# Kernel tuning notes

Measured on AMD Instinct MI355X. Metric: run time of the kernel, lower is better.

The kernel has to match this reference:

```python
import jax, jax.numpy as jnp
import numpy as np

B, N = 16, 512


def _line_coords(n):
    # Discrete Fourier slice coordinates for all mValues (center=False, ridgelet=False).
    mu = n + n // 2 if n % 2 == 0 else n + 1
    p = 2 if n % 2 == 0 else n
    m = jnp.arange(mu)           # [mu]
    k = jnp.arange(n)            # [N]
    lt = (m < n)[:, None]        # m < N branch mask, [mu, 1]
    # m < N:  row = k,                 col = (k*m) % N
    # m >= N: row = (k*p*(m-N)) % N,   col = k
    row = jnp.where(lt, k[None, :], (k[None, :] * p * (m[:, None] - n)) % n)
    col = jnp.where(lt, (k[None, :] * m[:, None]) % n, k[None, :])
    return row, col  # each [mu, N] int32


def setup_inputs() -> dict:
    key = jax.random.key(0)
    return {"image": jax.random.normal(key, (B, N, N), dtype=jnp.float32)}


def reference(image):
    b, n, _ = image.shape
    row, col = _line_coords(n)                                   # [mu, N]
    dft = jnp.fft.fft2(image.astype(jnp.complex64), norm="ortho")  # [B, N, N] c64
    slices = dft[:, row, col]                                    # gather -> [B, mu, N]
    sino = jnp.fft.ifft(slices, norm="ortho")                    # [B, mu, N] c64
    # complex sinogram returned as stacked (real, imag) float channels
    return jnp.stack([sino.real, sino.imag], axis=-1)            # [B, mu, N, 2]
```

## Files before the change

### kernel.cpp

```cpp
#include <hip/hip_runtime.h>
#include <hip/hip_fp16.h>


#define NN 512
#define MU 768
#define MASK 511
#define SCALE 0.04419417382415922f
#define NB 768

typedef float v4f __attribute__((ext_vector_type(4)));

union H8 { float4 f4; __half2 h2[4]; };
union H4 { float2 f2; __half2 h2[2]; };

__device__ __forceinline__ void gridbar(unsigned* cnt, unsigned target) {
  __syncthreads();
  if (threadIdx.x == 0) {
    __threadfence();
    atomicAdd(cnt, 1u);
    while (__atomic_load_n(cnt, __ATOMIC_ACQUIRE) < target)
      __builtin_amdgcn_s_sleep(8);
    __threadfence();
  }
  __syncthreads();
}

__global__ __launch_bounds__(512, 6) void drt_fused(
    const float* __restrict__ img, float2* __restrict__ out,
    __half* __restrict__ A0, __half* __restrict__ B0,
    __half* __restrict__ A1, __half* __restrict__ B1,
    unsigned* __restrict__ bar) {
  __shared__ float LDS[8320];
  const int bid = blockIdx.x;
  const int t = threadIdx.x;

  if (bid < 512) {
    const int b = bid >> 5, tile = bid & 31;
    const int xt = tile & 7, wt = tile >> 3;
    const int x0 = xt * 64, w0 = wt * 64, x3 = ((xt + 4) & 7) * 64;
    const float* src = img + (size_t)b * NN * NN;
    float* TA = LDS;
    float* TB = LDS + 4160;
    for (int idx = t; idx < 4096; idx += 512) {
      int rr = idx >> 6, cc = idx & 63;
      TA[rr * 65 + cc] = src[(x0 + rr) * NN + w0 + cc];
      TB[rr * 65 + cc] = src[(x0 + rr) * NN + w0 + 256 + cc];
    }
    __syncthreads();
    __half2* d = (__half2*)A0 + (size_t)b * 512 * 256;
    for (int idx = t; idx < 2048; idx += 512) {
      int wl = idx >> 5, xp = idx & 31;
      float a0 = TA[(2 * xp) * 65 + wl] + TB[(2 * xp) * 65 + wl];
      float a1 = TA[(2 * xp + 1) * 65 + wl] + TB[(2 * xp + 1) * 65 + wl];
      d[(w0 + wl) * 256 + (x0 >> 1) + xp] = __float22half2_rn(make_float2(a0, a1));
    }
    __syncthreads();
    for (int idx = t; idx < 4096; idx += 512) {
      int rr = idx >> 6, cc = idx & 63;
      TB[rr * 65 + cc] = src[(x3 + rr) * NN + w0 + 256 + cc];
    }
    __syncthreads();
    for (int idx = t; idx < 2048; idx += 512) {
      int wl = idx >> 5, xp = idx & 31;
      float a0 = TA[(2 * xp) * 65 + wl] + TB[(2 * xp) * 65 + wl];
      float a1 = TA[(2 * xp + 1) * 65 + wl] + TB[(2 * xp + 1) * 65 + wl];
      d[(256 + w0 + wl) * 256 + (x0 >> 1) + xp] = __float22half2_rn(make_float2(a0, a1));
    }
  } else {
    const int v = bid - 512, b = v >> 4, unit = v & 15;
    const int w0 = unit * 16;
    const float2* s2 = (const float2*)(img + (size_t)b * NN * NN);
    __half2* d = (__half2*)B0 + (size_t)b * 256 * 256;
    for (int it = 0; it < 8; ++it) {
      int flat = it * 512 + t;
      int row = w0 + (flat >> 8), cp = flat & 255;
      float2 u = s2[row * 256 + cp], vv = s2[(row + 256) * 256 + cp];
      d[row * 256 + cp] = __float22half2_rn(make_float2(u.x + vv.x, u.y + vv.y));
    }
  }

  gridbar(bar, NB);

  {
    const int b = bid / 48, bx = bid - b * 48;
    const bool isB = bx >= 32;
    const int c = isB ? 0 : (bx >> 4);
    const int w = isB ? (bx - 32) : (bx & 15);
    const __half* in = isB ? (B0 + (size_t)b * 256 * NN) : (A0 + (size_t)b * 512 * NN);
    const int pbase = c * 256 + w;
    float* L = LDS;
    const float4* s4 = (const float4*)in;
    for (int it = 0; it < 2; ++it) {
      int flat = it * 512 + t;
      int lrow = flat >> 6, ch = flat & 63;
      H8 u; u.f4 = s4[(size_t)(pbase + 16 * lrow) * 64 + ch];
      float2 p0 = __half22float2(u.h2[0]), p1 = __half22float2(u.h2[1]);
      float2 p2 = __half22float2(u.h2[2]), p3 = __half22float2(u.h2[3]);
      float4* l4 = (float4*)&L[lrow * 512 + ch * 8];
      l4[0] = make_float4(p0.x, p0.y, p1.x, p1.y);
      l4[1] = make_float4(p2.x, p2.y, p3.x, p3.y);
    }
    __syncthreads();
    const int g = t >> 7;
    const int x4 = (t & 127) * 4;
    __half* outA = A1 + (size_t)b * 512 * NN;
    __half* outB = B1 + (size_t)b * 256 * NN;
    for (int jj = 0; jj < 4; ++jj) {
      const int j = jj * 4 + g;
      const int C = isB ? (2 * j) : (c + 2 * j);
      float4 acc = {0.f, 0.f, 0.f, 0.f};
#pragma unroll
      for (int bb = 0; bb < 16; ++bb) {
        int base = (x4 - C * bb * 16) & MASK;
        float4 v = *(const float4*)&L[bb * 512 + base];
        acc.x += v.x; acc.y += v.y; acc.z += v.z; acc.w += v.w;
      }
      const int orow = isB ? (j * 16 + w) : (C * 16 + w);
      H4 h;
      h.h2[0] = __float22half2_rn(make_float2(acc.x, acc.y));
      h.h2[1] = __float22half2_rn(make_float2(acc.z, acc.w));
      float2* op = (float2*)(isB ? outB : outA);
      op[orow * 128 + (x4 >> 2)] = h.f2;
    }
  }

  gridbar(bar, 2 * NB);

  {
    const int b = bid / 48, bx = bid - b * 48;
    const bool isB = bx >= 32;
    const int c = isB ? 2 * (bx - 32) : bx;
    const __half* in = isB ? (B1 + (size_t)b * 256 * NN + (size_t)(bx - 32) * 16 * NN)
                           : (A1 + (size_t)b * 512 * NN + (size_t)c * 16 * NN);
    float* L = LDS;
    const __half2* i2 = (const __half2*)in;
    for (int it = 0; it < 8; ++it) {
      int flat = it * 512 + t;
      int bb = flat >> 8, p = flat & 255;
      float2 f = __half22float2(i2[bb * 256 + p]);
      int y0 = (2 * p + c * bb) & MASK;
      L[bb * 512 + y0] = f.x;
      L[bb * 512 + ((y0 + 1) & MASK)] = f.y;
    }
    __syncthreads();
    const int g = t >> 7;
    const int xq = (t & 127) << 2;
    float4 acc[4];
#pragma unroll
    for (int jj = 0; jj < 4; ++jj) acc[jj] = {0.f, 0.f, 0.f, 0.f};
#pragma unroll
    for (int bb = 0; bb < 16; ++bb) {
      const float* row = L + bb * 512;
      int base = (xq - 128 * g * bb) & MASK;
      const int step = (32 * bb) & MASK;
#pragma unroll
      for (int jj = 0; jj < 4; ++jj) {
        float4 v = *(const float4*)&row[base];
        acc[jj].x += v.x; acc[jj].y += v.y; acc[jj].z += v.z; acc[jj].w += v.w;
        base = (base - step) & MASK;
      }
    }
#pragma unroll
    for (int jj = 0; jj < 4; ++jj) {
      const int j = 4 * g + jj;
      const int m = isB ? (512 + (bx - 32) + 16 * j) : (c + 32 * j);
      v4f o1 = {acc[jj].x * SCALE, 0.f, acc[jj].y * SCALE, 0.f};
      v4f o2 = {acc[jj].z * SCALE, 0.f, acc[jj].w * SCALE, 0.f};
      v4f* op = (v4f*)(out + ((size_t)b * MU + m) * NN + xq);
      __builtin_nontemporal_store(o1, op);
      __builtin_nontemporal_store(o2, op + 1);
    }
  }
}

__global__ __launch_bounds__(256) void k_init(const float* __restrict__ img,
                                              float* __restrict__ A0,
                                              float* __restrict__ B0) {
  const int bx = blockIdx.x, b = blockIdx.y;
  const float* src = img + (size_t)b * NN * NN;
  if (bx < 32) {
    __shared__ float T1[64][65], T2[64][65], T3[64][65];
    const int xt = bx & 7, wt = bx >> 3;
    const int x0 = xt * 64, w0 = wt * 64, x3 = ((xt + 4) & 7) * 64;
    for (int idx = threadIdx.x; idx < 4096; idx += 256) {
      int rr = idx >> 6, cc = idx & 63;
      T1[rr][cc] = src[(x0 + rr) * NN + w0 + cc];
      T2[rr][cc] = src[(x0 + rr) * NN + w0 + 256 + cc];
      T3[rr][cc] = src[(x3 + rr) * NN + w0 + 256 + cc];
    }
    __syncthreads();
    float* dst = A0 + (size_t)b * (512 * NN);
    for (int idx = threadIdx.x; idx < 4096; idx += 256) {
      int wl = idx >> 6, xl = idx & 63;
      float t1 = T1[xl][wl];
      dst[(size_t)(w0 + wl) * NN + x0 + xl]       = t1 + T2[xl][wl];
      dst[(size_t)(256 + w0 + wl) * NN + x0 + xl] = t1 + T3[xl][wl];
    }
  } else {
    const int w0 = (bx - 32) * 32;
    const float4* s4 = (const float4*)src;
    float4* d4 = (float4*)(B0 + (size_t)b * (256 * NN));
    for (int it = 0; it < 16; ++it) {
      int flat = it * 256 + threadIdx.x;
      int row = w0 + (flat >> 7), col = flat & 127;
      float4 u = s4[row * 128 + col], v = s4[(row + 256) * 128 + col];
      u.x += v.x; u.y += v.y; u.z += v.z; u.w += v.w;
      d4[row * 128 + col] = u;
    }
  }
}

__global__ __launch_bounds__(512) void k_pass1(const float* __restrict__ A0,
                                               const float* __restrict__ B0,
                                               float* __restrict__ A1,
                                               float* __restrict__ B1) {
  __shared__ float L[16 * 512];
  const int bx = blockIdx.x, b = blockIdx.y;
  const int t = threadIdx.x;
  const bool isB = bx >= 32;
  const int c = isB ? 0 : (bx >> 4);
  const int w = isB ? (bx - 32) : (bx & 15);
  const float* in = isB ? (B0 + (size_t)b * 256 * NN) : (A0 + (size_t)b * 512 * NN);
  {
    const float4* s4 = (const float4*)in;
    float4* l4 = (float4*)L;
    const int pbase = c * 256 + w;
    for (int it = 0; it < 4; ++it) {
      int flat = it * 512 + t;
      int lrow = flat >> 7, col = flat & 127;
      l4[lrow * 128 + col] = s4[(pbase + 16 * lrow) * 128 + col];
    }
  }
  __syncthreads();
  const int g = t >> 7;
  const int x4 = (t & 127) * 4;
  float* outA = A1 + (size_t)b * 512 * NN;
  float* outB = B1 + (size_t)b * 256 * NN;
  for (int jj = 0; jj < 4; ++jj) {
    const int j = jj * 4 + g;
    const int C = isB ? (2 * j) : (c + 2 * j);
    float4 acc = {0.f, 0.f, 0.f, 0.f};
#pragma unroll
    for (int bb = 0; bb < 16; ++bb) {
      int base = (x4 - C * bb * 16) & MASK;
      float4 v = *(const float4*)&L[bb * 512 + base];
      acc.x += v.x; acc.y += v.y; acc.z += v.z; acc.w += v.w;
    }
    const int orow = isB ? (j * 16 + w) : (C * 16 + w);
    float* op = isB ? outB : outA;
    *(float4*)&op[(size_t)orow * NN + x4] = acc;
  }
}

__global__ __launch_bounds__(512) void k_pass2(const float* __restrict__ A1,
                                               const float* __restrict__ B1,
                                               float2* __restrict__ out) {
  __shared__ float L[16 * 512];
  const int bx = blockIdx.x, b = blockIdx.y;
  const int t = threadIdx.x;
  const bool isB = bx >= 32;
  const int c = isB ? 2 * (bx - 32) : bx;
  const float* in = isB ? (B1 + (size_t)b * 256 * NN + (size_t)(bx - 32) * 16 * NN)
                        : (A1 + (size_t)b * 512 * NN + (size_t)c * 16 * NN);
#pragma unroll
  for (int bb = 0; bb < 16; ++bb) {
    float v = in[bb * 512 + t];
    L[bb * 512 + ((t + c * bb) & MASK)] = v;
  }
  __syncthreads();
  const int g = t >> 7;
  const int xq = (t & 127) << 2;
  float4 acc[4];
#pragma unroll
  for (int jj = 0; jj < 4; ++jj) acc[jj] = {0.f, 0.f, 0.f, 0.f};
#pragma unroll
  for (int bb = 0; bb < 16; ++bb) {
    const float* row = L + bb * 512;
    int base = (xq - 128 * g * bb) & MASK;
    const int step = (32 * bb) & MASK;
#pragma unroll
    for (int jj = 0; jj < 4; ++jj) {
      float4 v = *(const float4*)&row[base];
      acc[jj].x += v.x; acc[jj].y += v.y; acc[jj].z += v.z; acc[jj].w += v.w;
      base = (base - step) & MASK;
    }
  }
#pragma unroll
  for (int jj = 0; jj < 4; ++jj) {
    const int j = 4 * g + jj;
    const int m = isB ? (512 + (bx - 32) + 16 * j) : (c + 32 * j);
    float2* op = out + ((size_t)b * MU + m) * NN + xq;
    float4 a = acc[jj];
    op[0] = {a.x * SCALE, 0.f};
    op[1] = {a.y * SCALE, 0.f};
    op[2] = {a.z * SCALE, 0.f};
    op[3] = {a.w * SCALE, 0.f};
  }
}

extern "C" void kernel_launch(void* const* d_in, const int* in_sizes, int n_in,
                              void* d_out, int out_size, void* d_ws, size_t ws_size,
                              hipStream_t stream) {
  const float* img = (const float*)d_in[0];

  int maxb = 0;
  (void)hipOccupancyMaxActiveBlocksPerMultiprocessor(&maxb, (const void*)drt_fused,
                                                     512, 0);
  const bool can_fuse = (maxb >= 3) && (ws_size >= (size_t)25165832);

  if (can_fuse) {
    char* W = (char*)d_ws;
    __half* A0 = (__half*)(W);
    __half* A1 = (__half*)(W + 8388608);
    __half* B0 = (__half*)(W + 16777216);
    __half* B1 = (__half*)(W + 20971520);
    unsigned* bar = (unsigned*)(W + 25165824);
    (void)hipMemsetAsync(bar, 0, 8, stream);
    drt_fused<<<dim3(NB), dim3(512), 0, stream>>>(img, (float2*)d_out,
                                                  A0, B0, A1, B1, bar);
  } else if (ws_size >= (size_t)51 * 1024 * 1024) {
    float* W  = (float*)d_ws;
    float* A0 = W;
    float* A1 = W + 4194304;
    float* B0 = W + 8388608;
    float* B1 = W + 10485760;
    k_init <<<dim3(40, 16), dim3(256), 0, stream>>>(img, A0, B0);
    k_pass1<<<dim3(48, 16), dim3(512), 0, stream>>>(A0, B0, A1, B1);
    k_pass2<<<dim3(48, 16), dim3(512), 0, stream>>>(A1, B1, (float2*)d_out);
  }
}
```

Baseline: 108.9 us.

## Replace grid-wide barriers with per-batch barriers and fuse B-path init into pass1

```diff
diff --git a/kernel.cpp b/kernel.cpp
--- a/kernel.cpp
+++ b/kernel.cpp
@@ -13,11 +13,15 @@
 union H8 { float4 f4; __half2 h2[4]; };
 union H4 { float2 f2; __half2 h2[2]; };
 
-__device__ __forceinline__ void gridbar(unsigned* cnt, unsigned target) {
+__device__ __forceinline__ void bar_signal(unsigned* cnt) {
   __syncthreads();
   if (threadIdx.x == 0) {
     __threadfence();
     atomicAdd(cnt, 1u);
+  }
+}
+__device__ __forceinline__ void bar_wait(unsigned* cnt, unsigned target) {
+  if (threadIdx.x == 0) {
     while (__atomic_load_n(cnt, __ATOMIC_ACQUIRE) < target)
       __builtin_amdgcn_s_sleep(8);
     __threadfence();
@@ -27,148 +31,209 @@
 
 __global__ __launch_bounds__(512, 6) void drt_fused(
     const float* __restrict__ img, float2* __restrict__ out,
-    __half* __restrict__ A0, __half* __restrict__ B0,
-    __half* __restrict__ A1, __half* __restrict__ B1,
-    unsigned* __restrict__ bar) {
-  __shared__ float LDS[8320];
+    __half* __restrict__ A0, __half* __restrict__ A1,
+    __half* __restrict__ B1, unsigned* __restrict__ bar) {
+  __shared__ float LDS[12480];
   const int bid = blockIdx.x;
   const int t = threadIdx.x;
+  unsigned* barA  = bar;
+  unsigned* barA2 = bar + 16;
+  unsigned* barB  = bar + 32;
 
   if (bid < 512) {
-    const int b = bid >> 5, tile = bid & 31;
-    const int xt = tile & 7, wt = tile >> 3;
-    const int x0 = xt * 64, w0 = wt * 64, x3 = ((xt + 4) & 7) * 64;
-    const float* src = img + (size_t)b * NN * NN;
-    float* TA = LDS;
-    float* TB = LDS + 4160;
-    for (int idx = t; idx < 4096; idx += 512) {
-      int rr = idx >> 6, cc = idx & 63;
-      TA[rr * 65 + cc] = src[(x0 + rr) * NN + w0 + cc];
-      TB[rr * 65 + cc] = src[(x0 + rr) * NN + w0 + 256 + cc];
-    }
-    __syncthreads();
-    __half2* d = (__half2*)A0 + (size_t)b * 512 * 256;
-    for (int idx = t; idx < 2048; idx += 512) {
-      int wl = idx >> 5, xp = idx & 31;
-      float a0 = TA[(2 * xp) * 65 + wl] + TB[(2 * xp) * 65 + wl];
-      float a1 = TA[(2 * xp + 1) * 65 + wl] + TB[(2 * xp + 1) * 65 + wl];
-      d[(w0 + wl) * 256 + (x0 >> 1) + xp] = __float22half2_rn(make_float2(a0, a1));
-    }
-    __syncthreads();
-    for (int idx = t; idx < 4096; idx += 512) {
-      int rr = idx >> 6, cc = idx & 63;
-      TB[rr * 65 + cc] = src[(x3 + rr) * NN + w0 + 256 + cc];
-    }
-    __syncthreads();
-    for (int idx = t; idx < 2048; idx += 512) {
-      int wl = idx >> 5, xp = idx & 31;
-      float a0 = TA[(2 * xp) * 65 + wl] + TB[(2 * xp) * 65 + wl];
-      float a1 = TA[(2 * xp + 1) * 65 + wl] + TB[(2 * xp + 1) * 65 + wl];
-      d[(256 + w0 + wl) * 256 + (x0 >> 1) + xp] = __float22half2_rn(make_float2(a0, a1));
+    const int b = bid >> 5, idx = bid & 31;
+
+    {
+      const int xt = idx & 7, wt = idx >> 3;
+      const int x0 = xt * 64, w0 = wt * 64, x3 = ((xt + 4) & 7) * 64;
+      const float* src = img + (size_t)b * NN * NN;
+      float* T1 = LDS;
+      float* T2 = LDS + 4160;
+      float* T3 = LDS + 8320;
+      for (int i = t; i < 4096; i += 512) {
+        int rr = i >> 6, cc = i & 63;
+        T1[rr * 65 + cc] = src[(x0 + rr) * NN + w0 + cc];
+        T2[rr * 65 + cc] = src[(x0 + rr) * NN + w0 + 256 + cc];
+        T3[rr * 65 + cc] = src[(x3 + rr) * NN + w0 + 256 + cc];
+      }
+      __syncthreads();
+      __half2* d = (__half2*)A0 + (size_t)b * 512 * 256;
+      for (int i = t; i < 2048; i += 512) {
+        int wl = i >> 5, xp = i & 31;
+        float t1a = T1[(2 * xp) * 65 + wl], t1b = T1[(2 * xp + 1) * 65 + wl];
+        float a0 = t1a + T2[(2 * xp) * 65 + wl];
+        float a1 = t1b + T2[(2 * xp + 1) * 65 + wl];
+        d[(w0 + wl) * 256 + (x0 >> 1) + xp] = __float22half2_rn(make_float2(a0, a1));
+        float b0 = t1a + T3[(2 * xp) * 65 + wl];
+        float b1 = t1b + T3[(2 * xp + 1) * 65 + wl];
+        d[(256 + w0 + wl) * 256 + (x0 >> 1) + xp] = __float22half2_rn(make_float2(b0, b1));
+      }
+    }
+
+    bar_signal(&barA[b]);
+    bar_wait(&barA[b], 32u);
+
+    {
+      const int c = idx >> 4, w = idx & 15;
+      float* L = LDS;
+      const float4* s4 = (const float4*)(A0 + (size_t)b * 512 * NN);
+      const int pbase = c * 256 + w;
+      for (int it = 0; it < 2; ++it) {
+        int flat = it * 512 + t;
+        int lrow = flat >> 6, ch = flat & 63;
+        H8 u; u.f4 = s4[(size_t)(pbase + 16 * lrow) * 64 + ch];
+        float2 p0 = __half22float2(u.h2[0]), p1 = __half22float2(u.h2[1]);
+        float2 p2 = __half22float2(u.h2[2]), p3 = __half22float2(u.h2[3]);
+        float4* l4 = (float4*)&L[lrow * 512 + ch * 8];
+        l4[0] = make_float4(p0.x, p0.y, p1.x, p1.y);
+        l4[1] = make_float4(p2.x, p2.y, p3.x, p3.y);
+      }
+      __syncthreads();
+      const int g = t >> 7;
+      const int x4 = (t & 127) * 4;
+      float2* op = (float2*)(A1 + (size_t)b * 512 * NN);
+      for (int jj = 0; jj < 4; ++jj) {
+        const int j = jj * 4 + g;
+        const int C = c + 2 * j;
+        float4 acc = {0.f, 0.f, 0.f, 0.f};
+#pragma unroll
+        for (int bb = 0; bb < 16; ++bb) {
+          int base = (x4 - C * bb * 16) & MASK;
+          float4 v = *(const float4*)&L[bb * 512 + base];
+          acc.x += v.x; acc.y += v.y; acc.z += v.z; acc.w += v.w;
+        }
+        H4 h;
+        h.h2[0] = __float22half2_rn(make_float2(acc.x, acc.y));
+        h.h2[1] = __float22half2_rn(make_float2(acc.z, acc.w));
+        op[(C * 16 + w) * 128 + (x4 >> 2)] = h.f2;
+      }
+    }
+
+    bar_signal(&barA2[b]);
+    bar_wait(&barA2[b], 32u);
+
+    {
+      const int c = idx;
+      const __half2* i2 = (const __half2*)(A1 + (size_t)b * 512 * NN +
+                                           (size_t)c * 16 * NN);
+      float* L = LDS;
+      for (int it = 0; it < 8; ++it) {
+        int flat = it * 512 + t;
+        int bb = flat >> 8, p = flat & 255;
+        float2 f = __half22float2(i2[bb * 256 + p]);
+        int y0 = (2 * p + c * bb) & MASK;
+        L[bb * 512 + y0] = f.x;
+        L[bb * 512 + ((y0 + 1) & MASK)] = f.y;
+      }
+      __syncthreads();
+      const int g = t >> 7;
+      const int xq = (t & 127) << 2;
+      float4 acc[4];
+#pragma unroll
+      for (int jj = 0; jj < 4; ++jj) acc[jj] = {0.f, 0.f, 0.f, 0.f};
+#pragma unroll
+      for (int bb = 0; bb < 16; ++bb) {
+        const float* row = L + bb * 512;
+        int base = (xq - 128 * g * bb) & MASK;
+        const int step = (32 * bb) & MASK;
+#pragma unroll
+        for (int jj = 0; jj < 4; ++jj) {
+          float4 v = *(const float4*)&row[base];
+          acc[jj].x += v.x; acc[jj].y += v.y; acc[jj].z += v.z; acc[jj].w += v.w;
+          base = (base - step) & MASK;
+        }
+      }
+#pragma unroll
+      for (int jj = 0; jj < 4; ++jj) {
+        const int j = 4 * g + jj;
+        const int m = c + 32 * j;
+        v4f o1 = {acc[jj].x * SCALE, 0.f, acc[jj].y * SCALE, 0.f};
+        v4f o2 = {acc[jj].z * SCALE, 0.f, acc[jj].w * SCALE, 0.f};
+        v4f* op = (v4f*)(out + ((size_t)b * MU + m) * NN + xq);
+        __builtin_nontemporal_store(o1, op);
+        __builtin_nontemporal_store(o2, op + 1);
+      }
     }
   } else {
-    const int v = bid - 512, b = v >> 4, unit = v & 15;
-    const int w0 = unit * 16;
-    const float2* s2 = (const float2*)(img + (size_t)b * NN * NN);
-    __half2* d = (__half2*)B0 + (size_t)b * 256 * 256;
-    for (int it = 0; it < 8; ++it) {
-      int flat = it * 512 + t;
-      int row = w0 + (flat >> 8), cp = flat & 255;
-      float2 u = s2[row * 256 + cp], vv = s2[(row + 256) * 256 + cp];
-      d[row * 256 + cp] = __float22half2_rn(make_float2(u.x + vv.x, u.y + vv.y));
-    }
-  }
-
-  gridbar(bar, NB);
-
-  {
-    const int b = bid / 48, bx = bid - b * 48;
-    const bool isB = bx >= 32;
-    const int c = isB ? 0 : (bx >> 4);
-    const int w = isB ? (bx - 32) : (bx & 15);
-    const __half* in = isB ? (B0 + (size_t)b * 256 * NN) : (A0 + (size_t)b * 512 * NN);
-    const int pbase = c * 256 + w;
-    float* L = LDS;
-    const float4* s4 = (const float4*)in;
-    for (int it = 0; it < 2; ++it) {
-      int flat = it * 512 + t;
-      int lrow = flat >> 6, ch = flat & 63;
-      H8 u; u.f4 = s4[(size_t)(pbase + 16 * lrow) * 64 + ch];
-      float2 p0 = __half22float2(u.h2[0]), p1 = __half22float2(u.h2[1]);
-      float2 p2 = __half22float2(u.h2[2]), p3 = __half22float2(u.h2[3]);
-      float4* l4 = (float4*)&L[lrow * 512 + ch * 8];
-      l4[0] = make_float4(p0.x, p0.y, p1.x, p1.y);
-      l4[1] = make_float4(p2.x, p2.y, p3.x, p3.y);
-    }
-    __syncthreads();
-    const int g = t >> 7;
-    const int x4 = (t & 127) * 4;
-    __half* outA = A1 + (size_t)b * 512 * NN;
-    __half* outB = B1 + (size_t)b * 256 * NN;
-    for (int jj = 0; jj < 4; ++jj) {
-      const int j = jj * 4 + g;
-      const int C = isB ? (2 * j) : (c + 2 * j);
-      float4 acc = {0.f, 0.f, 0.f, 0.f};
+    const int v = bid - 512, b = v >> 4, w = v & 15;
+
+    {
+      float* L = LDS;
+      const float4* s4 = (const float4*)(img + (size_t)b * NN * NN);
+      for (int it = 0; it < 4; ++it) {
+        int flat = it * 512 + t;
+        int lrow = flat >> 7, col = flat & 127;
+        float4 u = s4[(w + 16 * lrow) * 128 + col];
+        float4 z = s4[(w + 16 * lrow + 256) * 128 + col];
+        u.x += z.x; u.y += z.y; u.z += z.z; u.w += z.w;
+        *(float4*)&L[lrow * 512 + col * 4] = u;
+      }
+      __syncthreads();
+      const int g = t >> 7;
+      const int x4 = (t & 127) * 4;
+      float2* op = (float2*)(B1 + (size_t)b * 256 * NN);
+      for (int jj = 0; jj < 4; ++jj) {
+        const int j = jj * 4 + g;
+        const int C = 2 * j;
+        float4 acc = {0.f, 0.f, 0.f, 0.f};
+#pragma unroll
+        for (int bb = 0; bb < 16; ++bb) {
+          int base = (x4 - C * bb * 16) & MASK;
+          float4 vv = *(const float4*)&L[bb * 512 + base];
+          acc.x += vv.x; acc.y += vv.y; acc.z += vv.z; acc.w += vv.w;
+        }
+        H4 h;
+        h.h2[0] = __float22half2_rn(make_float2(acc.x, acc.y));
+        h.h2[1] = __float22half2_rn(make_float2(acc.z, acc.w));
+        op[(j * 16 + w) * 128 + (x4 >> 2)] = h.f2;
+      }
+    }
+
+    bar_signal(&barB[b]);
+    bar_wait(&barB[b], 16u);
+
+    {
+      const int a = w;
+      const int c = 2 * a;
+      const __half2* i2 = (const __half2*)(B1 + (size_t)b * 256 * NN +
+                                           (size_t)a * 16 * NN);
+      float* L = LDS;
+      for (int it = 0; it < 8; ++it) {
+        int flat = it * 512 + t;
+        int bb = flat >> 8, p = flat & 255;
+        float2 f = __half22float2(i2[bb * 256 + p]);
+        int y0 = (2 * p + c * bb) & MASK;
+        L[bb * 512 + y0] = f.x;
+        L[bb * 512 + ((y0 + 1) & MASK)] = f.y;
+      }
+      __syncthreads();
+      const int g = t >> 7;
+      const int xq = (t & 127) << 2;
+      float4 acc[4];
+#pragma unroll
+      for (int jj = 0; jj < 4; ++jj) acc[jj] = {0.f, 0.f, 0.f, 0.f};
 #pragma unroll
       for (int bb = 0; bb < 16; ++bb) {
-        int base = (x4 - C * bb * 16) & MASK;
-        float4 v = *(const float4*)&L[bb * 512 + base];
-        acc.x += v.x; acc.y += v.y; acc.z += v.z; acc.w += v.w;
-      }
-      const int orow = isB ? (j * 16 + w) : (C * 16 + w);
-      H4 h;
-      h.h2[0] = __float22half2_rn(make_float2(acc.x, acc.y));
-      h.h2[1] = __float22half2_rn(make_float2(acc.z, acc.w));
-      float2* op = (float2*)(isB ? outB : outA);
-      op[orow * 128 + (x4 >> 2)] = h.f2;
-    }
-  }
-
-  gridbar(bar, 2 * NB);
-
-  {
-    const int b = bid / 48, bx = bid - b * 48;
-    const bool isB = bx >= 32;
-    const int c = isB ? 2 * (bx - 32) : bx;
-    const __half* in = isB ? (B1 + (size_t)b * 256 * NN + (size_t)(bx - 32) * 16 * NN)
-                           : (A1 + (size_t)b * 512 * NN + (size_t)c * 16 * NN);
-    float* L = LDS;
-    const __half2* i2 = (const __half2*)in;
-    for (int it = 0; it < 8; ++it) {
-      int flat = it * 512 + t;
-      int bb = flat >> 8, p = flat & 255;
-      float2 f = __half22float2(i2[bb * 256 + p]);
-      int y0 = (2 * p + c * bb) & MASK;
-      L[bb * 512 + y0] = f.x;
-      L[bb * 512 + ((y0 + 1) & MASK)] = f.y;
-    }
-    __syncthreads();
-    const int g = t >> 7;
-    const int xq = (t & 127) << 2;
-    float4 acc[4];
-#pragma unroll
-    for (int jj = 0; jj < 4; ++jj) acc[jj] = {0.f, 0.f, 0.f, 0.f};
-#pragma unroll
-    for (int bb = 0; bb < 16; ++bb) {
-      const float* row = L + bb * 512;
-      int base = (xq - 128 * g * bb) & MASK;
-      const int step = (32 * bb) & MASK;
+        const float* row = L + bb * 512;
+        int base = (xq - 128 * g * bb) & MASK;
+        const int step = (32 * bb) & MASK;
+#pragma unroll
+        for (int jj = 0; jj < 4; ++jj) {
+          float4 vv = *(const float4*)&row[base];
+          acc[jj].x += vv.x; acc[jj].y += vv.y; acc[jj].z += vv.z; acc[jj].w += vv.w;
+          base = (base - step) & MASK;
+        }
+      }
 #pragma unroll
       for (int jj = 0; jj < 4; ++jj) {
-        float4 v = *(const float4*)&row[base];
-        acc[jj].x += v.x; acc[jj].y += v.y; acc[jj].z += v.z; acc[jj].w += v.w;
-        base = (base - step) & MASK;
-      }
-    }
-#pragma unroll
-    for (int jj = 0; jj < 4; ++jj) {
-      const int j = 4 * g + jj;
-      const int m = isB ? (512 + (bx - 32) + 16 * j) : (c + 32 * j);
-      v4f o1 = {acc[jj].x * SCALE, 0.f, acc[jj].y * SCALE, 0.f};
-      v4f o2 = {acc[jj].z * SCALE, 0.f, acc[jj].w * SCALE, 0.f};
-      v4f* op = (v4f*)(out + ((size_t)b * MU + m) * NN + xq);
-      __builtin_nontemporal_store(o1, op);
-      __builtin_nontemporal_store(o2, op + 1);
+        const int j = 4 * g + jj;
+        const int m = 512 + a + 16 * j;
+        v4f o1 = {acc[jj].x * SCALE, 0.f, acc[jj].y * SCALE, 0.f};
+        v4f o2 = {acc[jj].z * SCALE, 0.f, acc[jj].w * SCALE, 0.f};
+        v4f* op = (v4f*)(out + ((size_t)b * MU + m) * NN + xq);
+        __builtin_nontemporal_store(o1, op);
+        __builtin_nontemporal_store(o2, op + 1);
+      }
     }
   }
 }
@@ -306,18 +371,17 @@
   int maxb = 0;
   (void)hipOccupancyMaxActiveBlocksPerMultiprocessor(&maxb, (const void*)drt_fused,
                                                      512, 0);
-  const bool can_fuse = (maxb >= 3) && (ws_size >= (size_t)25165832);
+  const bool can_fuse = (maxb >= 3) && (ws_size >= (size_t)(20971520 + 192));
 
   if (can_fuse) {
     char* W = (char*)d_ws;
     __half* A0 = (__half*)(W);
     __half* A1 = (__half*)(W + 8388608);
-    __half* B0 = (__half*)(W + 16777216);
-    __half* B1 = (__half*)(W + 20971520);
-    unsigned* bar = (unsigned*)(W + 25165824);
-    (void)hipMemsetAsync(bar, 0, 8, stream);
+    __half* B1 = (__half*)(W + 16777216);
+    unsigned* bar = (unsigned*)(W + 20971520);
+    (void)hipMemsetAsync(bar, 0, 192, stream);
     drt_fused<<<dim3(NB), dim3(512), 0, stream>>>(img, (float2*)d_out,
-                                                  A0, B0, A1, B1, bar);
+                                                  A0, A1, B1, bar);
   } else if (ws_size >= (size_t)51 * 1024 * 1024) {
     float* W  = (float*)d_ws;
     float* A0 = W;
```

New measurement: 107.4 us. About the same (-1.4%).
